# Optimization experiments

Measured on AMD Instinct MI355X. Metric: run time of the kernel, lower is better.

Reference implementation:

```python
import jax, jax.numpy as jnp
import numpy as np

P = 16            # num_patches = 224 // 14
T = P * P         # patches per image (256)
K = 5             # top-k templates
SIM_THR = 0.05
PATCH_THR = 2.0


def _idx2loc(idx):
    # flat patch index -> (w, h) float location, matching convert_index2location
    return jnp.stack([(idx % P).astype(jnp.float32), (idx // P).astype(jnp.float32)], axis=-1)


def setup_inputs() -> dict:
    key = jax.random.key(0)
    k1, k2, k3, k4 = jax.random.split(key, 4)
    B, N, C = 8, 32, 768
    src_feats = jax.random.normal(k1, (B, N, C, P, P), dtype=jnp.float32)
    tar_feat = jax.random.normal(k2, (B, C, P, P), dtype=jnp.float32)
    src_masks = (jax.random.uniform(k3, (B, N, P, P)) > 0.3).astype(jnp.float32)
    tar_mask = (jax.random.uniform(k4, (B, P, P)) > 0.3).astype(jnp.float32)
    return {"src_feats": src_feats, "tar_feat": tar_feat,
            "src_masks": src_masks, "tar_mask": tar_mask}


def reference(src_feats, tar_feat, src_masks, tar_mask):
    B, N, C = src_feats.shape[:3]
    # masks are already at feature resolution -> interpolate is identity; flatten
    tarm = tar_mask.reshape(B, T)                                   # (B, T)
    srcm = src_masks.reshape(B, N, T)                               # (B, N, T)
    # L2-normalize features over channel dim (F.normalize)
    tf = tar_feat / jnp.clip(jnp.linalg.norm(tar_feat, axis=1, keepdims=True), 1e-12)
    tf = tf.reshape(B, C, T)                                        # (B, C, T)
    sf = src_feats / jnp.clip(jnp.linalg.norm(src_feats, axis=2, keepdims=True), 1e-12)
    sf = sf.reshape(B, N, C, T)                                     # (B, N, C, S)
    # dense cosine similarity, masked, then thresholded to 0
    sim = jnp.einsum('bct,bncs->bnts', tf, sf)                      # (B, N, T, S)
    sim = sim * srcm[:, :, None, :] * tarm[:, None, :, None]
    sim = jnp.where(sim < SIM_THR, 0.0, sim)
    # dual nearest-neighbor search ('tar2src' direction)
    score_t2s = sim.max(axis=3)                                     # (B, N, T)
    idx_t2s = sim.argmax(axis=3).astype(jnp.int32)
    score_s2t = sim.max(axis=2)                                     # (B, N, S)
    idx_s2t = sim.argmax(axis=2).astype(jnp.int32)
    mask_sim = score_t2s >= SIM_THR
    # cycle consistency: tar -> src -> tar
    idx_s2s = jnp.take_along_axis(idx_s2t, idx_t2s, axis=2)         # (B, N, T)
    dist = jnp.linalg.norm(_idx2loc(idx_s2s) - _idx2loc(jnp.arange(T))[None, None], axis=-1)
    sim_s2s = jnp.take_along_axis(score_s2t, idx_t2s, axis=2)
    mask_cycle = (dist <= PATCH_THR) & (sim_s2s >= SIM_THR)
    # non-zero / in-mask filtering
    mask_t2s = jnp.take_along_axis(srcm, idx_t2s, axis=2)           # (B, N, T)
    mask_nz = tarm[:, None, :] * mask_t2s * (idx_s2t != 0) * (idx_t2s != 0)
    mask_all = (mask_sim & mask_cycle) * mask_nz                    # (B, N, T) float
    match_counts = mask_all.sum(axis=2)                             # (B, N)
    sim_avg = jnp.where(match_counts > 0,
                        (score_t2s * mask_all).sum(axis=2) / float(T), 0.0)
    # top-k template selection
    score_src, id_src = jax.lax.top_k(sim_avg, K)                   # (B, K)
    sel = lambda a: jnp.take_along_axis(a, id_src[:, :, None], axis=1)
    pred_mask = sel(mask_all)                                       # (B, K, T)
    score_pts = sel(score_t2s)                                      # (B, K, T)
    src_loc = _idx2loc(sel(idx_t2s)).astype(jnp.int32)              # (B, K, T, 2)
    # format_prediction: -1 outside mask, (w, h) coords inside
    grid = _idx2loc(jnp.arange(T)).astype(jnp.int32)                # (T, 2)
    nz = (pred_mask != 0)[..., None]
    tar_pts = jnp.where(nz, grid[None, None], -1)                   # (B, K, T, 2)
    src_pts = jnp.where(nz, src_loc, -1)                            # (B, K, T, 2)
    return id_src, score_src, score_pts, tar_pts, src_pts, match_counts
```

## Files before the change

### kernel.cpp

```cpp
#include <hip/hip_runtime.h>

#define T_PATCH 256
#define C_DIM   768
#define NCH     48
#define N_B     8
#define N_N     32

typedef unsigned short u16;
typedef u16   u16x8  __attribute__((ext_vector_type(8)));
typedef u16   u16x4  __attribute__((ext_vector_type(4)));
typedef short s16x8  __attribute__((ext_vector_type(8)));
typedef float f32x16 __attribute__((ext_vector_type(16)));

__device__ __forceinline__ unsigned rne16(unsigned u) {
    return (u + 0x7fffu + ((u >> 16) & 1u)) >> 16;
}

__device__ __forceinline__ void split3(float x, u16& o0, u16& o1, u16& o2) {
    unsigned u0 = rne16(__float_as_uint(x));
    float f0 = __uint_as_float(u0 << 16);
    float r1 = x - f0;
    unsigned u1 = rne16(__float_as_uint(r1));
    float f1 = __uint_as_float(u1 << 16);
    float r2 = r1 - f1;
    o0 = (u16)u0; o1 = (u16)u1; o2 = (u16)(__float_as_uint(r2) >> 16);
}

__device__ __forceinline__ void gll16(const u16* g, u16* l) {
    __builtin_amdgcn_global_load_lds(
        (const __attribute__((address_space(1))) unsigned int*)g,
        (__attribute__((address_space(3))) unsigned int*)l, 16, 0, 0);
}

__global__ void tar_split_kernel(const float* __restrict__ tar,
                                 u16* __restrict__ tS0, u16* __restrict__ tS1,
                                 u16* __restrict__ tS2, float* __restrict__ partT) {
    int blk = blockIdx.x;
    int b = blk / NCH, c = blk - b * NCH;
    int tid = threadIdx.x;
    int g = tid >> 8, t = tid & 255;
    const float* tb = tar + (size_t)b * C_DIM * T_PATCH;
    float ss = 0.f;
    u16x8 v0, v1, v2;
    #pragma unroll
    for (int j = 0; j < 8; ++j) {
        float x = tb[(c * 16 + g * 8 + j) * T_PATCH + t];
        u16 a, bb, cc;
        split3(x, a, bb, cc);
        v0[j] = a; v1[j] = bb; v2[j] = cc;
        ss = fmaf(x, x, ss);
    }
    size_t off = ((size_t)blk * 512 + tid) * 8;
    *(u16x8*)(tS0 + off) = v0;
    *(u16x8*)(tS1 + off) = v1;
    *(u16x8*)(tS2 + off) = v2;
    __shared__ float sq[512];
    sq[tid] = ss;
    __syncthreads();
    if (tid < 256) partT[blk * 256 + tid] = sq[tid] + sq[tid + 256];
}

__launch_bounds__(512, 4)
__global__ void sim_kernel(const float* __restrict__ src_feats,
                           const u16* __restrict__ tS0, const u16* __restrict__ tS1,
                           const u16* __restrict__ tS2,
                           const float* __restrict__ partT,
                           const float* __restrict__ tar_mask,
                           const float* __restrict__ src_masks,
                           float* __restrict__ w_rowv, int* __restrict__ w_rowi,
                           float* __restrict__ w_s2tv, int* __restrict__ w_s2ti) {
    __shared__ __align__(16) u16 SM[36864];
    u16* Af0 = SM;
    u16* Af1 = SM + 8192;
    u16* Af2 = SM + 16384;
    u16* Bf0 = SM + 24576;
    u16* Bf1 = SM + 28672;
    u16* Bf2 = SM + 32768;
    float* sqv  = (float*)(SM);
    float* rowv = (float*)(SM + 1024);
    int*   rowi = (int*)  (SM + 3072);
    float* colv = (float*)(SM + 5120);
    int*   coli = (int*)  (SM + 6144);
    float* invT = (float*)(SM + 7168);
    float* invS = (float*)(SM + 7680);

    int bh = blockIdx.x;
    int b    = bh & 7;
    int loc  = bh >> 3;
    int n    = loc >> 1;
    int half = loc & 1;
    int bn   = b * N_N + n;
    int lbh  = bn * 2 + half;

    int tid = threadIdx.x;
    int lane = tid & 63, w = tid >> 6;
    int wm = w >> 1, wn = w & 1;
    int h = lane >> 5, l5 = lane & 31;
    int colB = tid & 127, qB = tid >> 7;
    int gq = qB >> 1, quad = qB & 1;

    const float* psrc = src_feats + (size_t)bn * C_DIM * T_PATCH
                      + (size_t)(gq * 8 + quad * 4) * T_PATCH + half * 128 + colB;
    size_t abase = (size_t)b * NCH * 4096 + (size_t)tid * 8;
    const u16* pga0 = tS0 + abase;
    const u16* pga1 = tS1 + abase;
    const u16* pga2 = tS2 + abase;

    f32x16 acc[2][2];
    #pragma unroll
    for (int i = 0; i < 2; ++i)
        #pragma unroll
        for (int j = 0; j < 2; ++j) acc[i][j] = (f32x16)0.0f;

    float sss = 0.f;

    {
        float yv[4];
        #pragma unroll
        for (int j = 0; j < 4; ++j) yv[j] = psrc[j * T_PATCH];
        psrc += 4096;
        gll16(pga0, Af0 + tid * 8);
        gll16(pga1, Af1 + tid * 8);
        gll16(pga2, Af2 + tid * 8);
        pga0 += 4096; pga1 += 4096; pga2 += 4096;
        u16x4 b0v, b1v, b2v;
        #pragma unroll
        for (int j = 0; j < 4; ++j) {
            u16 a, bb, cc;
            split3(yv[j], a, bb, cc);
            b0v[j] = a; b1v[j] = bb; b2v[j] = cc;
            sss = fmaf(yv[j], yv[j], sss);
        }
        int bslot = (gq * 128 + colB) * 8 + quad * 4;
        *(u16x4*)(Bf0 + bslot) = b0v;
        *(u16x4*)(Bf1 + bslot) = b1v;
        *(u16x4*)(Bf2 + bslot) = b2v;
    }
    __syncthreads();

    for (int c = 0; c < NCH; ++c) {
        int p = c & 1;
        bool pf = (c < NCH - 1);

        float yv[4];
        if (pf) {
            #pragma unroll
            for (int j = 0; j < 4; ++j) yv[j] = psrc[j * T_PATCH];
            psrc += 4096;
        }
        if (pf) {
            int adst = (p ^ 1) * 4096 + tid * 8;
            gll16(pga0, Af0 + adst);
            gll16(pga1, Af1 + adst);
            gll16(pga2, Af2 + adst);
            pga0 += 4096; pga1 += 4096; pga2 += 4096;
        }

        __builtin_amdgcn_s_setprio(1);
        s16x8 a0[2], a1[2], a2[2];
        {
            const u16* Ab = Af0 + p * 4096 + (h * 256 + wm * 64 + l5) * 8;
            #pragma unroll
            for (int i = 0; i < 2; ++i) a0[i] = *(const s16x8*)(Ab + i * 256);
            Ab = Af1 + p * 4096 + (h * 256 + wm * 64 + l5) * 8;
            #pragma unroll
            for (int i = 0; i < 2; ++i) a1[i] = *(const s16x8*)(Ab + i * 256);
            Ab = Af2 + p * 4096 + (h * 256 + wm * 64 + l5) * 8;
            #pragma unroll
            for (int i = 0; i < 2; ++i) a2[i] = *(const s16x8*)(Ab + i * 256);
        }
        #pragma unroll
        for (int j = 0; j < 2; ++j) {
            int boff = p * 2048 + (h * 128 + wn * 64 + j * 32 + l5) * 8;
            s16x8 b0 = *(const s16x8*)(Bf0 + boff);
            s16x8 b1 = *(const s16x8*)(Bf1 + boff);
            s16x8 b2 = *(const s16x8*)(Bf2 + boff);
            #pragma unroll
            for (int i = 0; i < 2; ++i) {
                acc[i][j] = __builtin_amdgcn_mfma_f32_32x32x16_bf16(a0[i], b0, acc[i][j], 0, 0, 0);
                acc[i][j] = __builtin_amdgcn_mfma_f32_32x32x16_bf16(a0[i], b1, acc[i][j], 0, 0, 0);
                acc[i][j] = __builtin_amdgcn_mfma_f32_32x32x16_bf16(a1[i], b0, acc[i][j], 0, 0, 0);
                acc[i][j] = __builtin_amdgcn_mfma_f32_32x32x16_bf16(a1[i], b1, acc[i][j], 0, 0, 0);
                acc[i][j] = __builtin_amdgcn_mfma_f32_32x32x16_bf16(a0[i], b2, acc[i][j], 0, 0, 0);
                acc[i][j] = __builtin_amdgcn_mfma_f32_32x32x16_bf16(a2[i], b0, acc[i][j], 0, 0, 0);
            }
        }
        __builtin_amdgcn_s_setprio(0);

        if (pf) {
            u16x4 b0v, b1v, b2v;
            #pragma unroll
            for (int j = 0; j < 4; ++j) {
                u16 a, bb, cc;
                split3(yv[j], a, bb, cc);
                b0v[j] = a; b1v[j] = bb; b2v[j] = cc;
                sss = fmaf(yv[j], yv[j], sss);
            }
            int bslot = (p ^ 1) * 2048 + (gq * 128 + colB) * 8 + quad * 4;
            *(u16x4*)(Bf0 + bslot) = b0v;
            *(u16x4*)(Bf1 + bslot) = b1v;
            *(u16x4*)(Bf2 + bslot) = b2v;
        }
        __syncthreads();
    }

    sqv[tid] = sss;
    if (tid < 256) {
        float s = 0.f;
        for (int c = 0; c < NCH; ++c) s += partT[(b * NCH + c) * 256 + tid];
        float tm = tar_mask[b * 256 + tid];
        invT[tid] = (tm != 0.f) ? 1.f / fmaxf(sqrtf(s), 1e-12f) : 0.f;
    }
    __syncthreads();
    if (tid < 128) {
        float ns = sqrtf(sqv[tid] + sqv[tid + 128] + sqv[tid + 256] + sqv[tid + 384]);
        float smv = src_masks[bn * 256 + half * 128 + tid];
        invS[tid] = (smv != 0.f) ? 1.f / fmaxf(ns, 1e-12f) : 0.f;
    }
    __syncthreads();

    float isv[2]; int sgl[2];
    #pragma unroll
    for (int j = 0; j < 2; ++j) {
        isv[j] = invS[wn * 64 + j * 32 + l5];
        sgl[j] = half * 128 + wn * 64 + j * 32 + l5;
    }
    float cbv[2]; int cbi[2];
    #pragma unroll
    for (int j = 0; j < 2; ++j) { cbv[j] = -1.f; cbi[j] = 0; }

    #pragma unroll
    for (int i = 0; i < 2; ++i) {
        #pragma unroll
        for (int r = 0; r < 16; ++r) {
            int trow = wm * 64 + i * 32 + (r & 3) + 8 * (r >> 2) + 4 * h;
            float it = invT[trow];
            float v[2];
            #pragma unroll
            for (int j = 0; j < 2; ++j) {
                float x = acc[i][j][r] * it * isv[j];
                v[j] = (x >= 0.05f) ? x : 0.f;
            }
            float bv = -1.f; int bi = 0;
            #pragma unroll
            for (int j = 0; j < 2; ++j)
                if (v[j] > bv) { bv = v[j]; bi = sgl[j]; }
            #pragma unroll
            for (int off = 1; off < 32; off <<= 1) {
                float ov = __shfl_xor(bv, off, 64);
                int   oi = __shfl_xor(bi, off, 64);
                if (ov > bv || (ov == bv && oi < bi)) { bv = ov; bi = oi; }
            }
            if (l5 == 0) { rowv[wn * 256 + trow] = bv; rowi[wn * 256 + trow] = bi; }
            #pragma unroll
            for (int j = 0; j < 2; ++j)
                if (v[j] > cbv[j]) { cbv[j] = v[j]; cbi[j] = trow; }
        }
    }
    #pragma unroll
    for (int j = 0; j < 2; ++j) {
        float bv = cbv[j]; int bi = cbi[j];
        float ov = __shfl_xor(bv, 32, 64);
        int   oi = __shfl_xor(bi, 32, 64);
        if (ov > bv || (ov == bv && oi < bi)) { bv = ov; bi = oi; }
        if (h == 0) { colv[wm * 128 + wn * 64 + j * 32 + l5] = bv;
                      coli[wm * 128 + wn * 64 + j * 32 + l5] = bi; }
    }
    __syncthreads();
    if (tid < 256) {
        float v0 = rowv[tid];       int i0 = rowi[tid];
        float v1 = rowv[256 + tid]; int i1 = rowi[256 + tid];
        if (v1 > v0 || (v1 == v0 && i1 < i0)) { v0 = v1; i0 = i1; }
        w_rowv[lbh * 256 + tid] = v0;
        w_rowi[lbh * 256 + tid] = i0;
    }
    if (tid < 128) {
        float bv = colv[tid]; int bi = coli[tid];
        #pragma unroll
        for (int q = 1; q < 4; ++q) {
            float ov = colv[q * 128 + tid]; int oi = coli[q * 128 + tid];
            if (ov > bv || (ov == bv && oi < bi)) { bv = ov; bi = oi; }
        }
        w_s2tv[bn * 256 + half * 128 + tid] = bv;
        w_s2ti[bn * 256 + half * 128 + tid] = bi;
    }
}

__launch_bounds__(1024)
__global__ void combine_final_kernel(const float* __restrict__ w_rowv,
                                     const int* __restrict__ w_rowi,
                                     const float* __restrict__ w_s2tv,
                                     const int* __restrict__ w_s2ti,
                                     const float* __restrict__ src_masks,
                                     const float* __restrict__ tar_mask,
                                     float* __restrict__ out) {
    int b   = blockIdx.x;
    int tid = threadIdx.x;
    int sub = tid >> 8;
    int t   = tid & 255;

    __shared__ float sc_s2t[4][256];
    __shared__ int   ix_s2t[4][256];
    __shared__ float sm[4][256];
    __shared__ float red[4][8];
    __shared__ float savg[32];
    __shared__ int   topid[5];
    __shared__ float topv[5];

    float tmv = tar_mask[b * 256 + t];

    for (int it = 0; it < 8; ++it) {
        int bnl = it * 4 + sub;
        int bn  = b * 32 + bnl;
        sc_s2t[sub][t] = w_s2tv[bn * 256 + t];
        ix_s2t[sub][t] = w_s2ti[bn * 256 + t];
        sm[sub][t]     = src_masks[bn * 256 + t];
        float v0 = w_rowv[(bn * 2) * 256 + t];     int i0 = w_rowi[(bn * 2) * 256 + t];
        float v1 = w_rowv[(bn * 2 + 1) * 256 + t]; int i1 = w_rowi[(bn * 2 + 1) * 256 + t];
        float st2s; int i;
        if (v1 > v0 || (v1 == v0 && i1 < i0)) { st2s = v1; i = i1; }
        else                                  { st2s = v0; i = i0; }
        __syncthreads();

        bool msim = st2s >= 0.05f;
        int is2s = ix_s2t[sub][i];
        int dw = (is2s & 15) - (t & 15);
        int dh = (is2s >> 4) - (t >> 4);
        bool cyc = (dw * dw + dh * dh <= 4) && (sc_s2t[sub][i] >= 0.05f);
        float mnz = tmv * sm[sub][i] *
                    ((ix_s2t[sub][t] != 0) ? 1.f : 0.f) *
                    ((i != 0) ? 1.f : 0.f);
        float mall = (msim && cyc) ? mnz : 0.f;

        float cnt = mall, svs = st2s * mall;
        #pragma unroll
        for (int off = 1; off < 64; off <<= 1) {
            cnt += __shfl_xor(cnt, off, 64);
            svs += __shfl_xor(svs, off, 64);
        }
        if ((t & 63) == 0) {
            red[sub][(t >> 6) * 2]     = cnt;
            red[sub][(t >> 6) * 2 + 1] = svs;
        }
        __syncthreads();
        if (t == 0) {
            float c = red[sub][0] + red[sub][2] + red[sub][4] + red[sub][6];
            float s = red[sub][1] + red[sub][3] + red[sub][5] + red[sub][7];
            savg[bnl] = (c > 0.f) ? (s * (1.f / 256.f)) : 0.f;
            out[51280 + bn] = c;
        }
        __syncthreads();
    }

    if (tid == 0) {
        unsigned used = 0;
        for (int k = 0; k < 5; ++k) {
            float bv = -1e30f; int bi = 0;
            for (int n = 0; n < 32; ++n) {
                if (!((used >> n) & 1u) && savg[n] > bv) { bv = savg[n]; bi = n; }
            }
            used |= (1u << bi);
            topid[k] = bi; topv[k] = bv;
        }
    }
    __syncthreads();
    if (tid < 5) {
        out[b * 5 + tid]      = (float)topid[tid];
        out[40 + b * 5 + tid] = topv[tid];
    }

    for (int kit = 0; kit < 2; ++kit) {
        int k = kit * 4 + sub;
        bool act = (k < 5);
        int bnl = act ? topid[k] : 0;
        int bn  = b * 32 + bnl;
        float st2s = 0.f; int i = 0;
        if (act) {
            sc_s2t[sub][t] = w_s2tv[bn * 256 + t];
            ix_s2t[sub][t] = w_s2ti[bn * 256 + t];
            sm[sub][t]     = src_masks[bn * 256 + t];
            float v0 = w_rowv[(bn * 2) * 256 + t];     int i0 = w_rowi[(bn * 2) * 256 + t];
            float v1 = w_rowv[(bn * 2 + 1) * 256 + t]; int i1 = w_rowi[(bn * 2 + 1) * 256 + t];
            if (v1 > v0 || (v1 == v0 && i1 < i0)) { st2s = v1; i = i1; }
            else                                  { st2s = v0; i = i0; }
        }
        __syncthreads();
        if (act) {
            bool msim = st2s >= 0.05f;
            int is2s = ix_s2t[sub][i];
            int dw = (is2s & 15) - (t & 15);
            int dh = (is2s >> 4) - (t >> 4);
            bool cyc = (dw * dw + dh * dh <= 4) && (sc_s2t[sub][i] >= 0.05f);
            float mnz = tmv * sm[sub][i] *
                        ((ix_s2t[sub][t] != 0) ? 1.f : 0.f) *
                        ((i != 0) ? 1.f : 0.f);
            float mall = (msim && cyc) ? mnz : 0.f;

            int o = (b * 5 + k) * 256 + t;
            out[80 + o] = st2s;
            bool nz = (mall != 0.f);
            out[10320 + 2 * o]     = nz ? (float)(t & 15) : -1.f;
            out[10320 + 2 * o + 1] = nz ? (float)(t >> 4) : -1.f;
            out[30800 + 2 * o]     = nz ? (float)(i & 15) : -1.f;
            out[30800 + 2 * o + 1] = nz ? (float)(i >> 4) : -1.f;
        }
        __syncthreads();
    }
}

extern "C" void kernel_launch(void* const* d_in, const int* in_sizes, int n_in,
                              void* d_out, int out_size, void* d_ws, size_t ws_size,
                              hipStream_t stream) {
    const float* src_feats = (const float*)d_in[0];
    const float* tar_feat  = (const float*)d_in[1];
    const float* src_masks = (const float*)d_in[2];
    const float* tar_mask  = (const float*)d_in[3];
    float* out = (float*)d_out;

    const size_t PLANE = (size_t)N_B * NCH * 512 * 8;
    u16* tS0 = (u16*)d_ws;
    u16* tS1 = tS0 + PLANE;
    u16* tS2 = tS1 + PLANE;
    float* partT  = (float*)(tS2 + PLANE);
    float* w_rowv = partT + (size_t)N_B * NCH * 256;
    int*   w_rowi = (int*)(w_rowv + 512 * 256);
    float* w_s2tv = (float*)(w_rowi + 512 * 256);
    int*   w_s2ti = (int*)(w_s2tv + 256 * 256);

    tar_split_kernel<<<N_B * NCH, 512, 0, stream>>>(tar_feat, tS0, tS1, tS2, partT);
    sim_kernel<<<N_B * N_N * 2, 512, 0, stream>>>(src_feats, tS0, tS1, tS2,
                                                  partT, tar_mask, src_masks,
                                                  w_rowv, w_rowi, w_s2tv, w_s2ti);
    combine_final_kernel<<<N_B, 1024, 0, stream>>>(w_rowv, w_rowi, w_s2tv, w_s2ti,
                                                   src_masks, tar_mask, out);
}
```

Before: 376.1 us.

## Deepen source prefetch to two chunks and stagger split/MFMA order across warps

The source feature loads are issued two chunks ahead through a second register buffer, so global latency has a full extra iteration to be hidden. Warps are split into two groups. Half run their MFMAs first and then split the prefetched source values into bf16 parts, while the other half split first and then run their MFMAs, so ALU and matrix work from different warps can overlap. This costs extra registers for the second buffer and duplicates code, which may lower occupancy.

```diff
diff --git a/kernel.cpp b/kernel.cpp
--- a/kernel.cpp
+++ b/kernel.cpp
@@ -114,10 +114,11 @@
 
     float sss = 0.f;
 
+    float yv[4], yv2[4];
     {
-        float yv[4];
-        #pragma unroll
-        for (int j = 0; j < 4; ++j) yv[j] = psrc[j * T_PATCH];
+        float y0[4];
+        #pragma unroll
+        for (int j = 0; j < 4; ++j) y0[j] = psrc[j * T_PATCH];
         psrc += 4096;
         gll16(pga0, Af0 + tid * 8);
         gll16(pga1, Af1 + tid * 8);
@@ -127,14 +128,17 @@
         #pragma unroll
         for (int j = 0; j < 4; ++j) {
             u16 a, bb, cc;
-            split3(yv[j], a, bb, cc);
+            split3(y0[j], a, bb, cc);
             b0v[j] = a; b1v[j] = bb; b2v[j] = cc;
-            sss = fmaf(yv[j], yv[j], sss);
+            sss = fmaf(y0[j], y0[j], sss);
         }
         int bslot = (gq * 128 + colB) * 8 + quad * 4;
         *(u16x4*)(Bf0 + bslot) = b0v;
         *(u16x4*)(Bf1 + bslot) = b1v;
         *(u16x4*)(Bf2 + bslot) = b2v;
+        #pragma unroll
+        for (int j = 0; j < 4; ++j) yv[j] = psrc[j * T_PATCH];
+        psrc += 4096;
     }
     __syncthreads();
 
@@ -142,10 +146,9 @@
         int p = c & 1;
         bool pf = (c < NCH - 1);
 
-        float yv[4];
-        if (pf) {
-            #pragma unroll
-            for (int j = 0; j < 4; ++j) yv[j] = psrc[j * T_PATCH];
+        if (c < NCH - 2) {
+            #pragma unroll
+            for (int j = 0; j < 4; ++j) yv2[j] = psrc[j * T_PATCH];
             psrc += 4096;
         }
         if (pf) {
@@ -156,51 +159,100 @@
             pga0 += 4096; pga1 += 4096; pga2 += 4096;
         }
 
-        __builtin_amdgcn_s_setprio(1);
-        s16x8 a0[2], a1[2], a2[2];
-        {
-            const u16* Ab = Af0 + p * 4096 + (h * 256 + wm * 64 + l5) * 8;
-            #pragma unroll
-            for (int i = 0; i < 2; ++i) a0[i] = *(const s16x8*)(Ab + i * 256);
-            Ab = Af1 + p * 4096 + (h * 256 + wm * 64 + l5) * 8;
-            #pragma unroll
-            for (int i = 0; i < 2; ++i) a1[i] = *(const s16x8*)(Ab + i * 256);
-            Ab = Af2 + p * 4096 + (h * 256 + wm * 64 + l5) * 8;
-            #pragma unroll
-            for (int i = 0; i < 2; ++i) a2[i] = *(const s16x8*)(Ab + i * 256);
-        }
-        #pragma unroll
-        for (int j = 0; j < 2; ++j) {
-            int boff = p * 2048 + (h * 128 + wn * 64 + j * 32 + l5) * 8;
-            s16x8 b0 = *(const s16x8*)(Bf0 + boff);
-            s16x8 b1 = *(const s16x8*)(Bf1 + boff);
-            s16x8 b2 = *(const s16x8*)(Bf2 + boff);
-            #pragma unroll
-            for (int i = 0; i < 2; ++i) {
-                acc[i][j] = __builtin_amdgcn_mfma_f32_32x32x16_bf16(a0[i], b0, acc[i][j], 0, 0, 0);
-                acc[i][j] = __builtin_amdgcn_mfma_f32_32x32x16_bf16(a0[i], b1, acc[i][j], 0, 0, 0);
-                acc[i][j] = __builtin_amdgcn_mfma_f32_32x32x16_bf16(a1[i], b0, acc[i][j], 0, 0, 0);
-                acc[i][j] = __builtin_amdgcn_mfma_f32_32x32x16_bf16(a1[i], b1, acc[i][j], 0, 0, 0);
-                acc[i][j] = __builtin_amdgcn_mfma_f32_32x32x16_bf16(a0[i], b2, acc[i][j], 0, 0, 0);
-                acc[i][j] = __builtin_amdgcn_mfma_f32_32x32x16_bf16(a2[i], b0, acc[i][j], 0, 0, 0);
-            }
-        }
-        __builtin_amdgcn_s_setprio(0);
-
-        if (pf) {
-            u16x4 b0v, b1v, b2v;
-            #pragma unroll
-            for (int j = 0; j < 4; ++j) {
-                u16 a, bb, cc;
-                split3(yv[j], a, bb, cc);
-                b0v[j] = a; b1v[j] = bb; b2v[j] = cc;
-                sss = fmaf(yv[j], yv[j], sss);
-            }
-            int bslot = (p ^ 1) * 2048 + (gq * 128 + colB) * 8 + quad * 4;
-            *(u16x4*)(Bf0 + bslot) = b0v;
-            *(u16x4*)(Bf1 + bslot) = b1v;
-            *(u16x4*)(Bf2 + bslot) = b2v;
-        }
+        if (w < 4) {
+            s16x8 a0[2], a1[2], a2[2];
+            {
+                const u16* Ab = Af0 + p * 4096 + (h * 256 + wm * 64 + l5) * 8;
+                #pragma unroll
+                for (int i = 0; i < 2; ++i) a0[i] = *(const s16x8*)(Ab + i * 256);
+                Ab = Af1 + p * 4096 + (h * 256 + wm * 64 + l5) * 8;
+                #pragma unroll
+                for (int i = 0; i < 2; ++i) a1[i] = *(const s16x8*)(Ab + i * 256);
+                Ab = Af2 + p * 4096 + (h * 256 + wm * 64 + l5) * 8;
+                #pragma unroll
+                for (int i = 0; i < 2; ++i) a2[i] = *(const s16x8*)(Ab + i * 256);
+            }
+            __builtin_amdgcn_s_setprio(1);
+            #pragma unroll
+            for (int j = 0; j < 2; ++j) {
+                int boff = p * 2048 + (h * 128 + wn * 64 + j * 32 + l5) * 8;
+                s16x8 b0 = *(const s16x8*)(Bf0 + boff);
+                s16x8 b1 = *(const s16x8*)(Bf1 + boff);
+                s16x8 b2 = *(const s16x8*)(Bf2 + boff);
+                #pragma unroll
+                for (int i = 0; i < 2; ++i) {
+                    acc[i][j] = __builtin_amdgcn_mfma_f32_32x32x16_bf16(a0[i], b0, acc[i][j], 0, 0, 0);
+                    acc[i][j] = __builtin_amdgcn_mfma_f32_32x32x16_bf16(a0[i], b1, acc[i][j], 0, 0, 0);
+                    acc[i][j] = __builtin_amdgcn_mfma_f32_32x32x16_bf16(a1[i], b0, acc[i][j], 0, 0, 0);
+                    acc[i][j] = __builtin_amdgcn_mfma_f32_32x32x16_bf16(a1[i], b1, acc[i][j], 0, 0, 0);
+                    acc[i][j] = __builtin_amdgcn_mfma_f32_32x32x16_bf16(a0[i], b2, acc[i][j], 0, 0, 0);
+                    acc[i][j] = __builtin_amdgcn_mfma_f32_32x32x16_bf16(a2[i], b0, acc[i][j], 0, 0, 0);
+                }
+            }
+            __builtin_amdgcn_s_setprio(0);
+            if (pf) {
+                u16x4 b0v, b1v, b2v;
+                #pragma unroll
+                for (int j = 0; j < 4; ++j) {
+                    u16 a, bb, cc;
+                    split3(yv[j], a, bb, cc);
+                    b0v[j] = a; b1v[j] = bb; b2v[j] = cc;
+                    sss = fmaf(yv[j], yv[j], sss);
+                }
+                int bslot = (p ^ 1) * 2048 + (gq * 128 + colB) * 8 + quad * 4;
+                *(u16x4*)(Bf0 + bslot) = b0v;
+                *(u16x4*)(Bf1 + bslot) = b1v;
+                *(u16x4*)(Bf2 + bslot) = b2v;
+            }
+        } else {
+            if (pf) {
+                u16x4 b0v, b1v, b2v;
+                #pragma unroll
+                for (int j = 0; j < 4; ++j) {
+                    u16 a, bb, cc;
+                    split3(yv[j], a, bb, cc);
+                    b0v[j] = a; b1v[j] = bb; b2v[j] = cc;
+                    sss = fmaf(yv[j], yv[j], sss);
+                }
+                int bslot = (p ^ 1) * 2048 + (gq * 128 + colB) * 8 + quad * 4;
+                *(u16x4*)(Bf0 + bslot) = b0v;
+                *(u16x4*)(Bf1 + bslot) = b1v;
+                *(u16x4*)(Bf2 + bslot) = b2v;
+            }
+            s16x8 a0[2], a1[2], a2[2];
+            {
+                const u16* Ab = Af0 + p * 4096 + (h * 256 + wm * 64 + l5) * 8;
+                #pragma unroll
+                for (int i = 0; i < 2; ++i) a0[i] = *(const s16x8*)(Ab + i * 256);
+                Ab = Af1 + p * 4096 + (h * 256 + wm * 64 + l5) * 8;
+                #pragma unroll
+                for (int i = 0; i < 2; ++i) a1[i] = *(const s16x8*)(Ab + i * 256);
+                Ab = Af2 + p * 4096 + (h * 256 + wm * 64 + l5) * 8;
+                #pragma unroll
+                for (int i = 0; i < 2; ++i) a2[i] = *(const s16x8*)(Ab + i * 256);
+            }
+            __builtin_amdgcn_s_setprio(1);
+            #pragma unroll
+            for (int j = 0; j < 2; ++j) {
+                int boff = p * 2048 + (h * 128 + wn * 64 + j * 32 + l5) * 8;
+                s16x8 b0 = *(const s16x8*)(Bf0 + boff);
+                s16x8 b1 = *(const s16x8*)(Bf1 + boff);
+                s16x8 b2 = *(const s16x8*)(Bf2 + boff);
+                #pragma unroll
+                for (int i = 0; i < 2; ++i) {
+                    acc[i][j] = __builtin_amdgcn_mfma_f32_32x32x16_bf16(a0[i], b0, acc[i][j], 0, 0, 0);
+                    acc[i][j] = __builtin_amdgcn_mfma_f32_32x32x16_bf16(a0[i], b1, acc[i][j], 0, 0, 0);
+                    acc[i][j] = __builtin_amdgcn_mfma_f32_32x32x16_bf16(a1[i], b0, acc[i][j], 0, 0, 0);
+                    acc[i][j] = __builtin_amdgcn_mfma_f32_32x32x16_bf16(a1[i], b1, acc[i][j], 0, 0, 0);
+                    acc[i][j] = __builtin_amdgcn_mfma_f32_32x32x16_bf16(a0[i], b2, acc[i][j], 0, 0, 0);
+                    acc[i][j] = __builtin_amdgcn_mfma_f32_32x32x16_bf16(a2[i], b0, acc[i][j], 0, 0, 0);
+                }
+            }
+            __builtin_amdgcn_s_setprio(0);
+        }
+
+        #pragma unroll
+        for (int j = 0; j < 4; ++j) yv[j] = yv2[j];
         __syncthreads();
     }
 
```

After: 449.1 us. 1.19x slower.
